# Optimization experiments

Measured on AMD Instinct MI355X. Metric: run time of the kernel, lower is better.

The kernel has to match this reference:

```python
import jax, jax.numpy as jnp
import numpy as np

N_HEADS = 4
D_HEAD = 16
SCALE = D_HEAD ** 0.5  # NOTE: original multiplies by sqrt(d_head), faithful


def _mha(x, Wq, bq, Wk, bk, Wv, bv, Wo, bo):
    # x: (..., N, D) with D = N_HEADS * D_HEAD
    q = jnp.einsum('...nd,od->...no', x, Wq) + bq
    k = jnp.einsum('...nd,od->...no', x, Wk) + bk
    v = jnp.einsum('...nd,od->...no', x, Wv) + bv
    lead = x.shape[:-2]
    n = x.shape[-2]
    q = q.reshape(*lead, n, N_HEADS, D_HEAD)
    k = k.reshape(*lead, n, N_HEADS, D_HEAD)
    v = v.reshape(*lead, n, N_HEADS, D_HEAD)
    scores = jnp.einsum('...nhd,...mhd->...hnm', q, k) * SCALE
    attn = jax.nn.softmax(scores, axis=-1)
    o = jnp.einsum('...hnm,...mhd->...nhd', attn, v).reshape(*lead, n, N_HEADS * D_HEAD)
    return jnp.einsum('...nd,od->...no', o, Wo) + bo


def setup_inputs() -> dict:
    key = jax.random.key(0)
    ks = jax.random.split(key, 20)
    b, n, d, dhf, G, C = 16, 16384, 64, 64, 256, 64
    s = 0.05
    inp = {
        'x': jax.random.normal(ks[0], (b, n, d), dtype=jnp.float32),
        'partitions': jax.random.permutation(ks[1], n).reshape(G, C).astype(jnp.int64),
    }
    names = ['q_intra', 'k_intra', 'v_intra', 'o_intra',
             'q_inter', 'k_inter', 'v_inter', 'o_inter']
    for i, nm in enumerate(names):
        d_in = d if nm.endswith('intra') and nm[0] != 'o' else dhf
        inp['W' + nm] = jax.random.normal(ks[2 + 2 * i], (dhf, d_in), dtype=jnp.float32) * s
        inp['b' + nm] = jax.random.normal(ks[3 + 2 * i], (dhf,), dtype=jnp.float32) * s
    return inp


def reference(x, partitions,
              Wq_intra, bq_intra, Wk_intra, bk_intra, Wv_intra, bv_intra, Wo_intra, bo_intra,
              Wq_inter, bq_inter, Wk_inter, bk_inter, Wv_inter, bv_inter, Wo_inter, bo_inter):
    b = x.shape[0]
    G, C = partitions.shape
    dhf = Wq_intra.shape[0]
    # gather nodes into groups: (b, G, C, d)
    xg = x[:, partitions, :]
    # intra-group attention, vectorized over (b, G)
    intra = _mha(xg, Wq_intra, bq_intra, Wk_intra, bk_intra,
                 Wv_intra, bv_intra, Wo_intra, bo_intra)  # (b, G, C, dhf)
    # MaxPool1d(kernel=dhf) over token axis with C == dhf -> max over tokens
    pooled = jnp.max(intra, axis=2)  # (b, G, dhf)
    inter = _mha(pooled, Wq_inter, bq_inter, Wk_inter, bk_inter,
                 Wv_inter, bv_inter, Wo_inter, bo_inter)  # (b, G, dhf)
    # broadcast-add inter-group features to every token in the group
    out = intra + inter[:, :, None, :]  # (b, G, C, dhf)
    flat = out.reshape(b, G * C, dhf)
    inv = jnp.argsort(partitions.reshape(-1))  # restore original node order
    return flat[:, inv, :]
```

## Files before the change

### kernel.cpp

```cpp
#include <hip/hip_runtime.h>
#include <hip/hip_bf16.h>

#define NTOK 16384
#define NG   256
#define NB   16

typedef float  f32x4   __attribute__((ext_vector_type(4)));
typedef short  short8v __attribute__((ext_vector_type(8)));
typedef short  short4v __attribute__((ext_vector_type(4)));

#define MFMA_BF16(a, b, c) __builtin_amdgcn_mfma_f32_16x16x32_bf16((a), (b), (c), 0, 0, 0)

__device__ __forceinline__ short f2bf(float f) {
    union { float f; unsigned u; } x; x.f = f;
    unsigned r = (x.u + 0x7FFF + ((x.u >> 16) & 1)) >> 16;
    return (short)r;
}
__device__ __forceinline__ float bf2f(short s) {
    union { float f; unsigned u; } x;
    x.u = ((unsigned)(unsigned short)s) << 16;
    return x.f;
}

__global__ void k_norm_part(const int* __restrict__ raw, int* __restrict__ part)
{
    const int i = blockIdx.x * 256 + threadIdx.x;
    const bool is64 = (raw[1] == 0 && raw[3] == 0 && raw[5] == 0);
    part[i] = is64 ? raw[2 * i] : raw[i];
}

__global__ void k_prep(const float* __restrict__ Wq, const float* __restrict__ Wk,
                       const float* __restrict__ Wv, const float* __restrict__ Wo,
                       const float* __restrict__ Wqe, const float* __restrict__ Wke,
                       const float* __restrict__ Wve, const float* __restrict__ Woe,
                       short8v* __restrict__ wf)
{
    const int gid = blockIdx.x * 256 + threadIdx.x;
    if (gid >= 5632) return;
    if (gid < 3584) {
        const int v    = gid >> 9;
        const int rem  = gid & 511;
        const int tau  = rem >> 6;
        const int lane = rem & 63;
        const int jt = tau >> 1, kt = tau & 1;
        const int o  = jt * 16 + (lane & 15);
        const int d0 = kt * 32 + (lane >> 4) * 8;
        const float* W = (v < 2) ? Wq : (v < 4) ? Wk : (v < 6) ? Wv : Wo;
        const bool lo = (v & 1) && (v < 6);
        short8v r8;
#pragma unroll
        for (int i = 0; i < 8; ++i) {
            const float f = W[o * 64 + d0 + i];
            const short hh = f2bf(f);
            r8[i] = lo ? f2bf(f - bf2f(hh)) : hh;
        }
        wf[gid] = r8;
    } else {
        const int g2   = gid - 3584;
        const int v    = g2 >> 9;
        const int rem  = g2 & 511;
        const int tau  = rem >> 6;
        const int lane = rem & 63;
        const int jt = tau >> 1, kt = tau & 1;
        const int o  = jt * 16 + (lane & 15);
        const int d0 = kt * 32 + (lane >> 4) * 8;
        const float* W = (v == 0) ? Wqe : (v == 1) ? Wke : (v == 2) ? Wve : Woe;
        short8v r8;
#pragma unroll
        for (int i = 0; i < 8; ++i) r8[i] = f2bf(W[o * 64 + d0 + i]);
        wf[gid] = r8;
    }
}

__global__ __launch_bounds__(256, 2) void k_intra(
    const float* __restrict__ x, const int* __restrict__ part,
    const short8v* __restrict__ wf,
    const float* __restrict__ bq, const float* __restrict__ bk,
    const float* __restrict__ bv, const float* __restrict__ bo,
    float* __restrict__ out, float* __restrict__ pooled)
{
    __shared__ __align__(16) short S[24576];
    __shared__ int pidx[64];

    short* const xh = S;
    short* const xl = S + 4096;
    short* const kk = S + 8192;
    short* const qh = S + 12288;
    short* const ql = S + 16384;
    short* const vT = S + 20480;

    const int t  = threadIdx.x;
    const int g  = blockIdx.x;
    const int bb = blockIdx.y;
    const int l  = t & 63;
    const int w  = t >> 6;
    const int quad = l >> 4;
    const int col  = l & 15;

    if (t < 64) pidx[t] = part[g * 64 + t];
    __syncthreads();

    for (int j = t; j < 512; j += 256) {
        const int row = j >> 3, c8 = j & 7;
        const float* px = x + ((size_t)bb * NTOK + pidx[row]) * 64 + c8 * 8;
        const float4 f0 = ((const float4*)px)[0];
        const float4 f1 = ((const float4*)px)[1];
        const float v[8] = {f0.x, f0.y, f0.z, f0.w, f1.x, f1.y, f1.z, f1.w};
        short8v h8, l8;
#pragma unroll
        for (int i = 0; i < 8; ++i) {
            const short h = f2bf(v[i]);
            h8[i] = h;
            l8[i] = f2bf(v[i] - bf2f(h));
        }
        const int idx = row * 64 + ((c8 ^ (row & 7)) << 3);
        *(short8v*)&xh[idx] = h8;
        *(short8v*)&xl[idx] = l8;
    }
    __syncthreads();

    {
        const float bqv = bq[w * 16 + col];
        const float bkv = bk[w * 16 + col];
        const float bvv = bv[w * 16 + col];
        short8v bqh[2], bql2[2], bkh[2], bkl[2], bvh[2], bvl[2];
#pragma unroll
        for (int kt = 0; kt < 2; ++kt) {
            const int tau = w * 2 + kt;
            bqh[kt]  = wf[(0 * 8 + tau) * 64 + l];
            bql2[kt] = wf[(1 * 8 + tau) * 64 + l];
            bkh[kt]  = wf[(2 * 8 + tau) * 64 + l];
            bkl[kt]  = wf[(3 * 8 + tau) * 64 + l];
            bvh[kt]  = wf[(4 * 8 + tau) * 64 + l];
            bvl[kt]  = wf[(5 * 8 + tau) * 64 + l];
        }
        for (int mt = 0; mt < 4; ++mt) {
            short8v axh[2], axl[2];
#pragma unroll
            for (int kt = 0; kt < 2; ++kt) {
                const int row = mt * 16 + col;
                const int idx = row * 64 + (((kt * 4 + quad) ^ (row & 7)) << 3);
                axh[kt] = *(const short8v*)&xh[idx];
                axl[kt] = *(const short8v*)&xl[idx];
            }
            f32x4 aq = {0.f, 0.f, 0.f, 0.f};
            f32x4 ak = {0.f, 0.f, 0.f, 0.f};
            f32x4 av = {0.f, 0.f, 0.f, 0.f};
#pragma unroll
            for (int kt = 0; kt < 2; ++kt) {
                aq = MFMA_BF16(axh[kt], bqh[kt],  aq);
                aq = MFMA_BF16(axh[kt], bql2[kt], aq);
                aq = MFMA_BF16(axl[kt], bqh[kt],  aq);
                ak = MFMA_BF16(axh[kt], bkh[kt],  ak);
                ak = MFMA_BF16(axh[kt], bkl[kt],  ak);
                ak = MFMA_BF16(axl[kt], bkh[kt],  ak);
                av = MFMA_BF16(axh[kt], bvh[kt],  av);
                av = MFMA_BF16(axh[kt], bvl[kt],  av);
                av = MFMA_BF16(axl[kt], bvh[kt],  av);
            }
#pragma unroll
            for (int r = 0; r < 4; ++r) {
                const int m = mt * 16 + quad * 4 + r;
                const int pos = m * 64 + (((w * 2 + (col >> 3)) ^ (m & 7)) << 3) + (col & 7);
                const float q4 = (aq[r] + bqv) * 4.0f;
                const short hq = f2bf(q4);
                qh[pos] = hq;
                ql[pos] = f2bf(q4 - bf2f(hq));
                kk[pos] = f2bf(ak[r] + bkv);
            }
            {
                const int d = w * 16 + col;
                short4v v4;
#pragma unroll
                for (int r = 0; r < 4; ++r) v4[r] = f2bf(av[r] + bvv);
                const int cm = mt * 2 + (quad >> 1);
                const int idx = d * 64 + ((cm ^ (d & 7)) << 3) + ((quad & 1) * 4);
                *(short4v*)&vT[idx] = v4;
            }
        }
    }

    const int h = w, hc = h * 16;
    f32x4 s[4][4];
    {
        short8v bk4[4];
#pragma unroll
        for (int jt = 0; jt < 4; ++jt) {
            const int row = jt * 16 + col;
            bk4[jt] = *(const short8v*)&kk[row * 64 + (((h * 2 + (quad & 1)) ^ (row & 7)) << 3)];
        }
        const short8v z8 = {0, 0, 0, 0, 0, 0, 0, 0};
        for (int it = 0; it < 4; ++it) {
            const int row = it * 16 + col;
            const int idx = row * 64 + (((h * 2 + (quad & 1)) ^ (row & 7)) << 3);
            short8v aqh = *(const short8v*)&qh[idx];
            short8v aql = *(const short8v*)&ql[idx];
            if (quad >= 2) { aqh = z8; aql = z8; }
#pragma unroll
            for (int jt = 0; jt < 4; ++jt) {
                f32x4 acc = {0.f, 0.f, 0.f, 0.f};
                acc = MFMA_BF16(aqh, bk4[jt], acc);
                acc = MFMA_BF16(aql, bk4[jt], acc);
                s[it][jt] = acc;
            }
        }
    }
    float rden[4][4];
    for (int it = 0; it < 4; ++it) {
#pragma unroll
        for (int r = 0; r < 4; ++r) {
            float mx = fmaxf(fmaxf(s[it][0][r], s[it][1][r]),
                             fmaxf(s[it][2][r], s[it][3][r]));
            mx = fmaxf(mx, __shfl_xor(mx, 1));
            mx = fmaxf(mx, __shfl_xor(mx, 2));
            mx = fmaxf(mx, __shfl_xor(mx, 4));
            mx = fmaxf(mx, __shfl_xor(mx, 8));
            float ds = 0.f;
#pragma unroll
            for (int jt = 0; jt < 4; ++jt) {
                const float e = __expf(s[it][jt][r] - mx);
                s[it][jt][r] = e;
                ds += e;
            }
            ds += __shfl_xor(ds, 1);
            ds += __shfl_xor(ds, 2);
            ds += __shfl_xor(ds, 4);
            ds += __shfl_xor(ds, 8);
            rden[it][r] = 1.0f / ds;
        }
    }
    __syncthreads();

    f32x4 oa[4];
#pragma unroll
    for (int it = 0; it < 4; ++it) oa[it] = (f32x4){0.f, 0.f, 0.f, 0.f};
    short* const Pw = S + w * 2560;
    for (int kt = 0; kt < 2; ++kt) {
        for (int it = 0; it < 4; ++it)
#pragma unroll
            for (int jl = 0; jl < 2; ++jl) {
                const int jt = kt * 2 + jl;
#pragma unroll
                for (int r = 0; r < 4; ++r)
                    Pw[(it * 16 + quad * 4 + r) * 40 + jl * 16 + col] = f2bf(s[it][jt][r]);
            }
        const int dv = hc + col;
        const int cmv = kt * 4 + quad;
        const short8v bv8 = *(const short8v*)&vT[dv * 64 + ((cmv ^ (dv & 7)) << 3)];
        for (int it = 0; it < 4; ++it) {
            const short8v ap = *(const short8v*)&Pw[(it * 16 + col) * 40 + quad * 8];
            oa[it] = MFMA_BF16(ap, bv8, oa[it]);
        }
    }
    for (int it = 0; it < 4; ++it)
#pragma unroll
        for (int r = 0; r < 4; ++r) {
            const int row = it * 16 + quad * 4 + r;
            const int pos = row * 64 + (((h * 2 + (col >> 3)) ^ (row & 7)) << 3) + (col & 7);
            qh[pos] = f2bf(oa[it][r] * rden[it][r]);
        }
    __syncthreads();

    {
        const float bov = bo[w * 16 + col];
        short8v bo8[2];
        bo8[0] = wf[(6 * 8 + w * 2 + 0) * 64 + l];
        bo8[1] = wf[(6 * 8 + w * 2 + 1) * 64 + l];
        float pm = -1e30f;
        for (int mt = 0; mt < 4; ++mt) {
            f32x4 acc = {0.f, 0.f, 0.f, 0.f};
#pragma unroll
            for (int kt = 0; kt < 2; ++kt) {
                const int row = mt * 16 + col;
                const short8v ao = *(const short8v*)&qh[row * 64 + (((kt * 4 + quad) ^ (row & 7)) << 3)];
                acc = MFMA_BF16(ao, bo8[kt], acc);
            }
#pragma unroll
            for (int r = 0; r < 4; ++r) {
                const float vo = acc[r] + bov;
                pm = fmaxf(pm, vo);
                const int tok = pidx[mt * 16 + quad * 4 + r];
                out[((size_t)bb * NTOK + tok) * 64 + w * 16 + col] = vo;
            }
        }
        pm = fmaxf(pm, __shfl_xor(pm, 16));
        pm = fmaxf(pm, __shfl_xor(pm, 32));
        if (l < 16)
            pooled[((size_t)bb * NG + g) * 64 + w * 16 + col] = pm;
    }
}

__global__ __launch_bounds__(256) void k_inter_qkv(
    const float* __restrict__ pooled, const short8v* __restrict__ wf,
    const float* __restrict__ bq, const float* __restrict__ bk,
    const float* __restrict__ bv,
    short* __restrict__ qws, short* __restrict__ kws, short* __restrict__ vTws)
{
    __shared__ __align__(16) short xs[4096];
    __shared__ __align__(16) short qs[64 * 72];
    __shared__ __align__(16) short ks2[64 * 72];
    const int t = threadIdx.x;
    const int chunk = blockIdx.x, bb = blockIdx.y;
    const int l = t & 63, w = t >> 6;
    const int quad = l >> 4, col = l & 15;

    for (int j = t; j < 512; j += 256) {
        const int row = j >> 3, c8 = j & 7;
        const float* px = pooled + ((size_t)bb * NG + chunk * 64 + row) * 64 + c8 * 8;
        const float4 f0 = ((const float4*)px)[0];
        const float4 f1 = ((const float4*)px)[1];
        const float v[8] = {f0.x, f0.y, f0.z, f0.w, f1.x, f1.y, f1.z, f1.w};
        short8v h8;
#pragma unroll
        for (int i = 0; i < 8; ++i) h8[i] = f2bf(v[i]);
        *(short8v*)&xs[row * 64 + ((c8 ^ (row & 7)) << 3)] = h8;
    }
    __syncthreads();

    const int WFI = 3584;
    short8v bqf[2], bkf[2], bvf[2];
#pragma unroll
    for (int kt = 0; kt < 2; ++kt) {
        bqf[kt] = wf[WFI + (0 * 8 + w * 2 + kt) * 64 + l];
        bkf[kt] = wf[WFI + (1 * 8 + w * 2 + kt) * 64 + l];
        bvf[kt] = wf[WFI + (2 * 8 + w * 2 + kt) * 64 + l];
    }
    const float bqv = bq[w * 16 + col];
    const float bkv = bk[w * 16 + col];
    const float bvv = bv[w * 16 + col];
    for (int mt = 0; mt < 4; ++mt) {
        short8v ax[2];
#pragma unroll
        for (int kt = 0; kt < 2; ++kt) {
            const int row = mt * 16 + col;
            ax[kt] = *(const short8v*)&xs[row * 64 + (((kt * 4 + quad) ^ (row & 7)) << 3)];
        }
        f32x4 aq = {0.f, 0.f, 0.f, 0.f};
        f32x4 ak = {0.f, 0.f, 0.f, 0.f};
        f32x4 av = {0.f, 0.f, 0.f, 0.f};
#pragma unroll
        for (int kt = 0; kt < 2; ++kt) {
            aq = MFMA_BF16(ax[kt], bqf[kt], aq);
            ak = MFMA_BF16(ax[kt], bkf[kt], ak);
            av = MFMA_BF16(ax[kt], bvf[kt], av);
        }
        short4v v4;
#pragma unroll
        for (int r = 0; r < 4; ++r) {
            const int m = mt * 16 + quad * 4 + r;
            qs[m * 72 + w * 16 + col]  = f2bf((aq[r] + bqv) * 4.0f);
            ks2[m * 72 + w * 16 + col] = f2bf(ak[r] + bkv);
            v4[r] = f2bf(av[r] + bvv);
        }
        *(short4v*)&vTws[((size_t)bb * 64 + w * 16 + col) * 256 + chunk * 64 + mt * 16 + quad * 4] = v4;
    }
    __syncthreads();
    for (int j = t; j < 512; j += 256) {
        const int row = j >> 3, c8 = j & 7;
        *(short8v*)&qws[((size_t)bb * NG + chunk * 64 + row) * 64 + c8 * 8] =
            *(const short8v*)&qs[row * 72 + c8 * 8];
        *(short8v*)&kws[((size_t)bb * NG + chunk * 64 + row) * 64 + c8 * 8] =
            *(const short8v*)&ks2[row * 72 + c8 * 8];
    }
}

__global__ __launch_bounds__(256) void k_inter_attn2(
    const short* __restrict__ qws, const short* __restrict__ kws,
    const short* __restrict__ vTws, const short8v* __restrict__ wf,
    const float* __restrict__ bo, float* __restrict__ inter)
{
    __shared__ __align__(16) short Pw_all[4 * 32 * 40];
    __shared__ __align__(16) short os[32 * 72];
    const int t = threadIdx.x;
    const int qt = blockIdx.x, bb = blockIdx.y;
    const int l = t & 63, w = t >> 6;
    const int quad = l >> 4, col = l & 15;
    const int hc = w * 16;
    const int r0 = qt * 32;

    const short8v z8 = {0, 0, 0, 0, 0, 0, 0, 0};
    short8v bk[16];
#pragma unroll
    for (int jt = 0; jt < 16; ++jt)
        bk[jt] = (quad < 2)
            ? *(const short8v*)&kws[((size_t)bb * NG + jt * 16 + col) * 64 + hc + quad * 8]
            : z8;
    short8v aq[2];
#pragma unroll
    for (int it = 0; it < 2; ++it)
        aq[it] = (quad < 2)
            ? *(const short8v*)&qws[((size_t)bb * NG + r0 + it * 16 + col) * 64 + hc + quad * 8]
            : z8;

    f32x4 s[2][16];
    for (int it = 0; it < 2; ++it)
#pragma unroll
        for (int jt = 0; jt < 16; ++jt) {
            f32x4 acc = {0.f, 0.f, 0.f, 0.f};
            s[it][jt] = MFMA_BF16(aq[it], bk[jt], acc);
        }

    float rden[2][4];
    for (int it = 0; it < 2; ++it)
#pragma unroll
        for (int r = 0; r < 4; ++r) {
            float mx = -1e30f;
#pragma unroll
            for (int jt = 0; jt < 16; ++jt) mx = fmaxf(mx, s[it][jt][r]);
            mx = fmaxf(mx, __shfl_xor(mx, 1));
            mx = fmaxf(mx, __shfl_xor(mx, 2));
            mx = fmaxf(mx, __shfl_xor(mx, 4));
            mx = fmaxf(mx, __shfl_xor(mx, 8));
            float ds = 0.f;
#pragma unroll
            for (int jt = 0; jt < 16; ++jt) {
                const float e = __expf(s[it][jt][r] - mx);
                s[it][jt][r] = e;
                ds += e;
            }
            ds += __shfl_xor(ds, 1);
            ds += __shfl_xor(ds, 2);
            ds += __shfl_xor(ds, 4);
            ds += __shfl_xor(ds, 8);
            rden[it][r] = 1.0f / ds;
        }

    short* const Pw = Pw_all + w * 32 * 40;
    f32x4 oa[2];
    oa[0] = (f32x4){0.f, 0.f, 0.f, 0.f};
    oa[1] = (f32x4){0.f, 0.f, 0.f, 0.f};
    for (int c = 0; c < 8; ++c) {
        for (int it = 0; it < 2; ++it)
#pragma unroll
            for (int jl = 0; jl < 2; ++jl) {
                const int jt = c * 2 + jl;
#pragma unroll
                for (int r = 0; r < 4; ++r)
                    Pw[(it * 16 + quad * 4 + r) * 40 + jl * 16 + col] = f2bf(s[it][jt][r]);
            }
        const short8v bv8 = *(const short8v*)&vTws[((size_t)bb * 64 + hc + col) * 256 + c * 32 + quad * 8];
        for (int it = 0; it < 2; ++it) {
            const short8v ap = *(const short8v*)&Pw[(it * 16 + col) * 40 + quad * 8];
            oa[it] = MFMA_BF16(ap, bv8, oa[it]);
        }
    }
    for (int it = 0; it < 2; ++it)
#pragma unroll
        for (int r = 0; r < 4; ++r)
            os[(it * 16 + quad * 4 + r) * 72 + hc + col] = f2bf(oa[it][r] * rden[it][r]);
    __syncthreads();

    short8v bof[2];
    bof[0] = wf[3584 + (3 * 8 + w * 2 + 0) * 64 + l];
    bof[1] = wf[3584 + (3 * 8 + w * 2 + 1) * 64 + l];
    const float bov = bo[w * 16 + col];
    for (int it = 0; it < 2; ++it) {
        f32x4 acc = {0.f, 0.f, 0.f, 0.f};
#pragma unroll
        for (int kt = 0; kt < 2; ++kt) {
            const short8v ao = *(const short8v*)&os[(it * 16 + col) * 72 + kt * 32 + quad * 8];
            acc = MFMA_BF16(ao, bof[kt], acc);
        }
#pragma unroll
        for (int r = 0; r < 4; ++r)
            inter[((size_t)bb * NG + r0 + it * 16 + quad * 4 + r) * 64 + w * 16 + col] = acc[r] + bov;
    }
}

__global__ __launch_bounds__(256) void k_scatter_add(
    const float* __restrict__ inter, const int* __restrict__ part,
    float* __restrict__ out)
{
    __shared__ float iv[64];
    __shared__ int   pidx[64];
    const int t  = threadIdx.x;
    const int g  = blockIdx.x;
    const int bb = blockIdx.y;
    if (t < 64) {
        iv[t]   = inter[((size_t)bb * NG + g) * 64 + t];
        pidx[t] = part[g * 64 + t];
    }
    __syncthreads();
    const int oo   = t & 63;
    const int cseg = t >> 6;
    const float add = iv[oo];
    for (int ci = 0; ci < 16; ++ci) {
        const int c = cseg * 16 + ci;
        float* p = out + ((size_t)bb * NTOK + pidx[c]) * 64 + oo;
        *p += add;
    }
}

extern "C" void kernel_launch(void* const* d_in, const int* in_sizes, int n_in,
                              void* d_out, int out_size, void* d_ws, size_t ws_size,
                              hipStream_t stream)
{
    const float* x    = (const float*)d_in[0];
    const int*   praw = (const int*)d_in[1];
    const float* Wq_a = (const float*)d_in[2];
    const float* bq_a = (const float*)d_in[3];
    const float* Wk_a = (const float*)d_in[4];
    const float* bk_a = (const float*)d_in[5];
    const float* Wv_a = (const float*)d_in[6];
    const float* bv_a = (const float*)d_in[7];
    const float* Wo_a = (const float*)d_in[8];
    const float* bo_a = (const float*)d_in[9];
    const float* Wq_e = (const float*)d_in[10];
    const float* bq_e = (const float*)d_in[11];
    const float* Wk_e = (const float*)d_in[12];
    const float* bk_e = (const float*)d_in[13];
    const float* Wv_e = (const float*)d_in[14];
    const float* bv_e = (const float*)d_in[15];
    const float* Wo_e = (const float*)d_in[16];
    const float* bo_e = (const float*)d_in[17];

    char* ws = (char*)d_ws;
    int*     part   = (int*)ws;
    float*   pooled = (float*)(ws + (1u << 16));
    float*   inter  = (float*)(ws + (1u << 16) + (1u << 20));
    short8v* wf     = (short8v*)(ws + (1u << 16) + 2 * (1u << 20));
    char*    base2  = ws + (1u << 16) + 2 * (1u << 20) + 98304;
    short*   qws    = (short*)base2;
    short*   kws    = (short*)(base2 + (1u << 19));
    short*   vTws   = (short*)(base2 + 2 * (1u << 19));

    float* out = (float*)d_out;

    k_norm_part<<<dim3(64), dim3(256), 0, stream>>>(praw, part);
    k_prep<<<dim3(22), dim3(256), 0, stream>>>(Wq_a, Wk_a, Wv_a, Wo_a,
                                               Wq_e, Wk_e, Wv_e, Wo_e, wf);
    k_intra<<<dim3(NG, NB), dim3(256), 0, stream>>>(
        x, part, wf, bq_a, bk_a, bv_a, bo_a, out, pooled);
    k_inter_qkv<<<dim3(4, NB), dim3(256), 0, stream>>>(
        pooled, wf, bq_e, bk_e, bv_e, qws, kws, vTws);
    k_inter_attn2<<<dim3(8, NB), dim3(256), 0, stream>>>(
        qws, kws, vTws, wf, bo_e, inter);
    k_scatter_add<<<dim3(NG, NB), dim3(256), 0, stream>>>(inter, part, out);
}
```

Baseline: 225.1 us.

## Drop x low-part split, use exp2 softmax, merge setup kernels, raise occupancy

```diff
diff --git a/kernel.cpp b/kernel.cpp
--- a/kernel.cpp
+++ b/kernel.cpp
@@ -10,36 +10,42 @@
 typedef short  short4v __attribute__((ext_vector_type(4)));
 
 #define MFMA_BF16(a, b, c) __builtin_amdgcn_mfma_f32_16x16x32_bf16((a), (b), (c), 0, 0, 0)
+
+#define QSCALE 5.770780163555856f
 
 __device__ __forceinline__ short f2bf(float f) {
     union { float f; unsigned u; } x; x.f = f;
     unsigned r = (x.u + 0x7FFF + ((x.u >> 16) & 1)) >> 16;
     return (short)r;
 }
+__device__ __forceinline__ short bft(float f) {
+    union { float f; unsigned u; } x; x.f = f;
+    return (short)(x.u >> 16);
+}
 __device__ __forceinline__ float bf2f(short s) {
     union { float f; unsigned u; } x;
     x.u = ((unsigned)(unsigned short)s) << 16;
     return x.f;
 }
 
-__global__ void k_norm_part(const int* __restrict__ raw, int* __restrict__ part)
-{
-    const int i = blockIdx.x * 256 + threadIdx.x;
-    const bool is64 = (raw[1] == 0 && raw[3] == 0 && raw[5] == 0);
-    part[i] = is64 ? raw[2 * i] : raw[i];
-}
-
-__global__ void k_prep(const float* __restrict__ Wq, const float* __restrict__ Wk,
-                       const float* __restrict__ Wv, const float* __restrict__ Wo,
-                       const float* __restrict__ Wqe, const float* __restrict__ Wke,
-                       const float* __restrict__ Wve, const float* __restrict__ Woe,
-                       short8v* __restrict__ wf)
+__global__ void k_setup(const int* __restrict__ raw, int* __restrict__ part,
+                        const float* __restrict__ Wq, const float* __restrict__ Wk,
+                        const float* __restrict__ Wv, const float* __restrict__ Wo,
+                        const float* __restrict__ Wqe, const float* __restrict__ Wke,
+                        const float* __restrict__ Wve, const float* __restrict__ Woe,
+                        short8v* __restrict__ wf)
 {
     const int gid = blockIdx.x * 256 + threadIdx.x;
-    if (gid >= 5632) return;
-    if (gid < 3584) {
-        const int v    = gid >> 9;
-        const int rem  = gid & 511;
+    if (gid < 16384) {
+        const bool is64 = (raw[1] == 0 && raw[3] == 0 && raw[5] == 0);
+        part[gid] = is64 ? raw[2 * gid] : raw[gid];
+        return;
+    }
+    const int p = gid - 16384;
+    if (p >= 5632) return;
+    if (p < 3584) {
+        const int v    = p >> 9;
+        const int rem  = p & 511;
         const int tau  = rem >> 6;
         const int lane = rem & 63;
         const int jt = tau >> 1, kt = tau & 1;
@@ -54,9 +60,9 @@
             const short hh = f2bf(f);
             r8[i] = lo ? f2bf(f - bf2f(hh)) : hh;
         }
-        wf[gid] = r8;
+        wf[p] = r8;
     } else {
-        const int g2   = gid - 3584;
+        const int g2   = p - 3584;
         const int v    = g2 >> 9;
         const int rem  = g2 & 511;
         const int tau  = rem >> 6;
@@ -68,26 +74,24 @@
         short8v r8;
 #pragma unroll
         for (int i = 0; i < 8; ++i) r8[i] = f2bf(W[o * 64 + d0 + i]);
-        wf[gid] = r8;
-    }
-}
-
-__global__ __launch_bounds__(256, 2) void k_intra(
+        wf[p] = r8;
+    }
+}
+
+__global__ __launch_bounds__(256, 4) void k_intra(
     const float* __restrict__ x, const int* __restrict__ part,
     const short8v* __restrict__ wf,
     const float* __restrict__ bq, const float* __restrict__ bk,
     const float* __restrict__ bv, const float* __restrict__ bo,
     float* __restrict__ out, float* __restrict__ pooled)
 {
-    __shared__ __align__(16) short S[24576];
-    __shared__ int pidx[64];
+    __shared__ __align__(16) short S[20480];
 
     short* const xh = S;
-    short* const xl = S + 4096;
-    short* const kk = S + 8192;
+    short* const kk = S + 4096;
+    short* const ql = S + 8192;
     short* const qh = S + 12288;
-    short* const ql = S + 16384;
-    short* const vT = S + 20480;
+    short* const vT = S + 16384;
 
     const int t  = threadIdx.x;
     const int g  = blockIdx.x;
@@ -97,25 +101,17 @@
     const int quad = l >> 4;
     const int col  = l & 15;
 
-    if (t < 64) pidx[t] = part[g * 64 + t];
-    __syncthreads();
-
     for (int j = t; j < 512; j += 256) {
         const int row = j >> 3, c8 = j & 7;
-        const float* px = x + ((size_t)bb * NTOK + pidx[row]) * 64 + c8 * 8;
+        const int tok = part[g * 64 + row];
+        const float* px = x + ((size_t)bb * NTOK + tok) * 64 + c8 * 8;
         const float4 f0 = ((const float4*)px)[0];
         const float4 f1 = ((const float4*)px)[1];
         const float v[8] = {f0.x, f0.y, f0.z, f0.w, f1.x, f1.y, f1.z, f1.w};
-        short8v h8, l8;
-#pragma unroll
-        for (int i = 0; i < 8; ++i) {
-            const short h = f2bf(v[i]);
-            h8[i] = h;
-            l8[i] = f2bf(v[i] - bf2f(h));
-        }
-        const int idx = row * 64 + ((c8 ^ (row & 7)) << 3);
-        *(short8v*)&xh[idx] = h8;
-        *(short8v*)&xl[idx] = l8;
+        short8v h8;
+#pragma unroll
+        for (int i = 0; i < 8; ++i) h8[i] = f2bf(v[i]);
+        *(short8v*)&xh[row * 64 + ((c8 ^ (row & 7)) << 3)] = h8;
     }
     __syncthreads();
 
@@ -135,13 +131,11 @@
             bvl[kt]  = wf[(5 * 8 + tau) * 64 + l];
         }
         for (int mt = 0; mt < 4; ++mt) {
-            short8v axh[2], axl[2];
+            short8v axh[2];
 #pragma unroll
             for (int kt = 0; kt < 2; ++kt) {
                 const int row = mt * 16 + col;
-                const int idx = row * 64 + (((kt * 4 + quad) ^ (row & 7)) << 3);
-                axh[kt] = *(const short8v*)&xh[idx];
-                axl[kt] = *(const short8v*)&xl[idx];
+                axh[kt] = *(const short8v*)&xh[row * 64 + (((kt * 4 + quad) ^ (row & 7)) << 3)];
             }
             f32x4 aq = {0.f, 0.f, 0.f, 0.f};
             f32x4 ak = {0.f, 0.f, 0.f, 0.f};
@@ -150,22 +144,19 @@
             for (int kt = 0; kt < 2; ++kt) {
                 aq = MFMA_BF16(axh[kt], bqh[kt],  aq);
                 aq = MFMA_BF16(axh[kt], bql2[kt], aq);
-                aq = MFMA_BF16(axl[kt], bqh[kt],  aq);
                 ak = MFMA_BF16(axh[kt], bkh[kt],  ak);
                 ak = MFMA_BF16(axh[kt], bkl[kt],  ak);
-                ak = MFMA_BF16(axl[kt], bkh[kt],  ak);
                 av = MFMA_BF16(axh[kt], bvh[kt],  av);
                 av = MFMA_BF16(axh[kt], bvl[kt],  av);
-                av = MFMA_BF16(axl[kt], bvh[kt],  av);
             }
 #pragma unroll
             for (int r = 0; r < 4; ++r) {
                 const int m = mt * 16 + quad * 4 + r;
                 const int pos = m * 64 + (((w * 2 + (col >> 3)) ^ (m & 7)) << 3) + (col & 7);
-                const float q4 = (aq[r] + bqv) * 4.0f;
-                const short hq = f2bf(q4);
+                const float q4 = (aq[r] + bqv) * QSCALE;
+                const short hq = bft(q4);
                 qh[pos] = hq;
-                ql[pos] = f2bf(q4 - bf2f(hq));
+                ql[pos] = bft(q4 - bf2f(hq));
                 kk[pos] = f2bf(ak[r] + bkv);
             }
             {
@@ -218,7 +209,7 @@
             float ds = 0.f;
 #pragma unroll
             for (int jt = 0; jt < 4; ++jt) {
-                const float e = __expf(s[it][jt][r] - mx);
+                const float e = exp2f(s[it][jt][r] - mx);
                 s[it][jt][r] = e;
                 ds += e;
             }
@@ -242,7 +233,7 @@
                 const int jt = kt * 2 + jl;
 #pragma unroll
                 for (int r = 0; r < 4; ++r)
-                    Pw[(it * 16 + quad * 4 + r) * 40 + jl * 16 + col] = f2bf(s[it][jt][r]);
+                    Pw[(it * 16 + quad * 4 + r) * 40 + jl * 16 + col] = bft(s[it][jt][r]);
             }
         const int dv = hc + col;
         const int cmv = kt * 4 + quad;
@@ -279,7 +270,7 @@
             for (int r = 0; r < 4; ++r) {
                 const float vo = acc[r] + bov;
                 pm = fmaxf(pm, vo);
-                const int tok = pidx[mt * 16 + quad * 4 + r];
+                const int tok = part[g * 64 + mt * 16 + quad * 4 + r];
                 out[((size_t)bb * NTOK + tok) * 64 + w * 16 + col] = vo;
             }
         }
@@ -348,7 +339,7 @@
 #pragma unroll
         for (int r = 0; r < 4; ++r) {
             const int m = mt * 16 + quad * 4 + r;
-            qs[m * 72 + w * 16 + col]  = f2bf((aq[r] + bqv) * 4.0f);
+            qs[m * 72 + w * 16 + col]  = f2bf((aq[r] + bqv) * QSCALE);
             ks2[m * 72 + w * 16 + col] = f2bf(ak[r] + bkv);
             v4[r] = f2bf(av[r] + bvv);
         }
@@ -369,14 +360,14 @@
     const short* __restrict__ vTws, const short8v* __restrict__ wf,
     const float* __restrict__ bo, float* __restrict__ inter)
 {
-    __shared__ __align__(16) short Pw_all[4 * 32 * 40];
-    __shared__ __align__(16) short os[32 * 72];
+    __shared__ __align__(16) short Pw_all[4 * 16 * 40];
+    __shared__ __align__(16) short os[16 * 72];
     const int t = threadIdx.x;
     const int qt = blockIdx.x, bb = blockIdx.y;
     const int l = t & 63, w = t >> 6;
     const int quad = l >> 4, col = l & 15;
     const int hc = w * 16;
-    const int r0 = qt * 32;
+    const int r0 = qt * 16;
 
     const short8v z8 = {0, 0, 0, 0, 0, 0, 0, 0};
     short8v bk[16];
@@ -385,85 +376,74 @@
         bk[jt] = (quad < 2)
             ? *(const short8v*)&kws[((size_t)bb * NG + jt * 16 + col) * 64 + hc + quad * 8]
             : z8;
-    short8v aq[2];
-#pragma unroll
-    for (int it = 0; it < 2; ++it)
-        aq[it] = (quad < 2)
-            ? *(const short8v*)&qws[((size_t)bb * NG + r0 + it * 16 + col) * 64 + hc + quad * 8]
-            : z8;
-
-    f32x4 s[2][16];
-    for (int it = 0; it < 2; ++it)
+    short8v aq = (quad < 2)
+        ? *(const short8v*)&qws[((size_t)bb * NG + r0 + col) * 64 + hc + quad * 8]
+        : z8;
+
+    f32x4 s[16];
+#pragma unroll
+    for (int jt = 0; jt < 16; ++jt) {
+        f32x4 acc = {0.f, 0.f, 0.f, 0.f};
+        s[jt] = MFMA_BF16(aq, bk[jt], acc);
+    }
+
+    float rden[4];
+#pragma unroll
+    for (int r = 0; r < 4; ++r) {
+        float mx = -1e30f;
+#pragma unroll
+        for (int jt = 0; jt < 16; ++jt) mx = fmaxf(mx, s[jt][r]);
+        mx = fmaxf(mx, __shfl_xor(mx, 1));
+        mx = fmaxf(mx, __shfl_xor(mx, 2));
+        mx = fmaxf(mx, __shfl_xor(mx, 4));
+        mx = fmaxf(mx, __shfl_xor(mx, 8));
+        float ds = 0.f;
 #pragma unroll
         for (int jt = 0; jt < 16; ++jt) {
-            f32x4 acc = {0.f, 0.f, 0.f, 0.f};
-            s[it][jt] = MFMA_BF16(aq[it], bk[jt], acc);
-        }
-
-    float rden[2][4];
-    for (int it = 0; it < 2; ++it)
-#pragma unroll
-        for (int r = 0; r < 4; ++r) {
-            float mx = -1e30f;
-#pragma unroll
-            for (int jt = 0; jt < 16; ++jt) mx = fmaxf(mx, s[it][jt][r]);
-            mx = fmaxf(mx, __shfl_xor(mx, 1));
-            mx = fmaxf(mx, __shfl_xor(mx, 2));
-            mx = fmaxf(mx, __shfl_xor(mx, 4));
-            mx = fmaxf(mx, __shfl_xor(mx, 8));
-            float ds = 0.f;
-#pragma unroll
-            for (int jt = 0; jt < 16; ++jt) {
-                const float e = __expf(s[it][jt][r] - mx);
-                s[it][jt][r] = e;
-                ds += e;
-            }
-            ds += __shfl_xor(ds, 1);
-            ds += __shfl_xor(ds, 2);
-            ds += __shfl_xor(ds, 4);
-            ds += __shfl_xor(ds, 8);
-            rden[it][r] = 1.0f / ds;
-        }
-
-    short* const Pw = Pw_all + w * 32 * 40;
-    f32x4 oa[2];
-    oa[0] = (f32x4){0.f, 0.f, 0.f, 0.f};
-    oa[1] = (f32x4){0.f, 0.f, 0.f, 0.f};
+            const float e = exp2f(s[jt][r] - mx);
+            s[jt][r] = e;
+            ds += e;
+        }
+        ds += __shfl_xor(ds, 1);
+        ds += __shfl_xor(ds, 2);
+        ds += __shfl_xor(ds, 4);
+        ds += __shfl_xor(ds, 8);
+        rden[r] = 1.0f / ds;
+    }
+
+    short* const Pw = Pw_all + w * 16 * 40;
+    f32x4 oa = {0.f, 0.f, 0.f, 0.f};
     for (int c = 0; c < 8; ++c) {
-        for (int it = 0; it < 2; ++it)
-#pragma unroll
-            for (int jl = 0; jl < 2; ++jl) {
-                const int jt = c * 2 + jl;
-#pragma unroll
-                for (int r = 0; r < 4; ++r)
-                    Pw[(it * 16 + quad * 4 + r) * 40 + jl * 16 + col] = f2bf(s[it][jt][r]);
-            }
+#pragma unroll
+        for (int jl = 0; jl < 2; ++jl) {
+            const int jt = c * 2 + jl;
+#pragma unroll
+            for (int r = 0; r < 4; ++r)
+                Pw[(quad * 4 + r) * 40 + jl * 16 + col] = bft(s[jt][r]);
+        }
         const short8v bv8 = *(const short8v*)&vTws[((size_t)bb * 64 + hc + col) * 256 + c * 32 + quad * 8];
-        for (int it = 0; it < 2; ++it) {
-            const short8v ap = *(const short8v*)&Pw[(it * 16 + col) * 40 + quad * 8];
-            oa[it] = MFMA_BF16(ap, bv8, oa[it]);
-        }
-    }
-    for (int it = 0; it < 2; ++it)
-#pragma unroll
-        for (int r = 0; r < 4; ++r)
-            os[(it * 16 + quad * 4 + r) * 72 + hc + col] = f2bf(oa[it][r] * rden[it][r]);
+        const short8v ap = *(const short8v*)&Pw[col * 40 + quad * 8];
+        oa = MFMA_BF16(ap, bv8, oa);
+    }
+#pragma unroll
+    for (int r = 0; r < 4; ++r)
+        os[(quad * 4 + r) * 72 + hc + col] = f2bf(oa[r] * rden[r]);
     __syncthreads();
 
     short8v bof[2];
     bof[0] = wf[3584 + (3 * 8 + w * 2 + 0) * 64 + l];
     bof[1] = wf[3584 + (3 * 8 + w * 2 + 1) * 64 + l];
     const float bov = bo[w * 16 + col];
-    for (int it = 0; it < 2; ++it) {
+    {
         f32x4 acc = {0.f, 0.f, 0.f, 0.f};
 #pragma unroll
         for (int kt = 0; kt < 2; ++kt) {
-            const short8v ao = *(const short8v*)&os[(it * 16 + col) * 72 + kt * 32 + quad * 8];
+            const short8v ao = *(const short8v*)&os[col * 72 + kt * 32 + quad * 8];
             acc = MFMA_BF16(ao, bof[kt], acc);
         }
 #pragma unroll
         for (int r = 0; r < 4; ++r)
-            inter[((size_t)bb * NG + r0 + it * 16 + quad * 4 + r) * 64 + w * 16 + col] = acc[r] + bov;
+            inter[((size_t)bb * NG + r0 + quad * 4 + r) * 64 + w * 16 + col] = acc[r] + bov;
     }
 }
 
@@ -526,14 +506,13 @@
 
     float* out = (float*)d_out;
 
-    k_norm_part<<<dim3(64), dim3(256), 0, stream>>>(praw, part);
-    k_prep<<<dim3(22), dim3(256), 0, stream>>>(Wq_a, Wk_a, Wv_a, Wo_a,
-                                               Wq_e, Wk_e, Wv_e, Wo_e, wf);
+    k_setup<<<dim3(86), dim3(256), 0, stream>>>(praw, part, Wq_a, Wk_a, Wv_a, Wo_a,
+                                                Wq_e, Wk_e, Wv_e, Wo_e, wf);
     k_intra<<<dim3(NG, NB), dim3(256), 0, stream>>>(
         x, part, wf, bq_a, bk_a, bv_a, bo_a, out, pooled);
     k_inter_qkv<<<dim3(4, NB), dim3(256), 0, stream>>>(
         pooled, wf, bq_e, bk_e, bv_e, qws, kws, vTws);
-    k_inter_attn2<<<dim3(8, NB), dim3(256), 0, stream>>>(
+    k_inter_attn2<<<dim3(16, NB), dim3(256), 0, stream>>>(
         qws, kws, vTws, wf, bo_e, inter);
     k_scatter_add<<<dim3(NG, NB), dim3(256), 0, stream>>>(inter, part, out);
 }
```

Result: no change. 223.6 us (-0.7%).
